# Performance work log

Measured on AMD Instinct MI355X. Metric: run time of the kernel, lower is better.

The kernel has to match this reference:

```python
import jax, jax.numpy as jnp
import numpy as np

N = 100000  # nodes
E = 1600000  # edges

def gcn_layer(x, W, b, src, tgt, ew):
    # support = x @ W + b ; messages gathered at src, weighted scatter-sum into tgt
    h = x @ W + b                      # [N, F_out]
    msg = h[src] * ew[:, None]         # [E, F_out]
    return jax.ops.segment_sum(msg, tgt, num_segments=N)  # [N, F_out]

def setup_inputs() -> dict:
    key = jax.random.key(0)
    ks = jax.random.split(key, 12)
    nfeat, nhid, nclass = 256, 128, 40
    x = jax.random.normal(ks[0], (N, nfeat), dtype=jnp.float32)
    src = jax.random.randint(ks[1], (E,), 0, N)
    tgt = jax.random.randint(ks[2], (E,), 0, N)
    edge_weight = jax.random.uniform(ks[3], (E,), dtype=jnp.float32)
    def w(k, fi, fo):
        return jax.random.normal(k, (fi, fo), dtype=jnp.float32) / np.sqrt(fi)
    return {
        "x": x, "src": src, "tgt": tgt, "edge_weight": edge_weight,
        "W0": w(ks[4], nfeat, nhid), "b0": jnp.zeros((nhid,), jnp.float32),
        "W1": w(ks[5], nhid, nhid),  "b1": jnp.zeros((nhid,), jnp.float32),
        "W2": w(ks[6], nhid, nhid),  "b2": jnp.zeros((nhid,), jnp.float32),
        "W3": w(ks[7], nhid, nclass),"b3": jnp.zeros((nclass,), jnp.float32),
    }

def reference(x, src, tgt, edge_weight, W0, b0, W1, b1, W2, b2, W3, b3):
    # RESK2 with nlayers=4, eval mode (dropout = identity).
    # x0 = relu(gc0); r = x0; x1 = relu(gc1); x2 = relu(gc2) + r; out = log_softmax(gc3)
    x0 = jax.nn.relu(gcn_layer(x, W0, b0, src, tgt, edge_weight))
    r = x0
    x1 = jax.nn.relu(gcn_layer(x0, W1, b1, src, tgt, edge_weight))
    x2 = jax.nn.relu(gcn_layer(x1, W2, b2, src, tgt, edge_weight)) + r
    logits = gcn_layer(x2, W3, b3, src, tgt, edge_weight)
    return jax.nn.log_softmax(logits, axis=1)
```

## Files before the change

kernel.cpp:

```cpp
#include <hip/hip_runtime.h>
#include <hip/hip_bf16.h>


typedef __attribute__((ext_vector_type(8))) short short8;
typedef __attribute__((ext_vector_type(4))) float float4v;

#define SC_SHIFT 8
#define SC_NODES 256
#define FILL_CAP 12288
#define SRC_MASK 0x1FFFF

static __device__ __forceinline__ float bf2f_lo(unsigned int v) {
    return __uint_as_float(v << 16);
}
static __device__ __forceinline__ float bf2f_hi(unsigned int v) {
    return __uint_as_float(v & 0xffff0000u);
}
static __device__ __forceinline__ unsigned short f2bf(float f) {
    unsigned int u = __float_as_uint(f);
    u = (u + 0x7fffu + ((u >> 16) & 1u)) >> 16;
    return (unsigned short)u;
}
static __device__ __forceinline__ unsigned int packbf(float a, float b) {
    return (unsigned int)f2bf(a) | ((unsigned int)f2bf(b) << 16);
}
static __device__ __forceinline__ float pw_w(unsigned int pe) {
    return __uint_as_float((pe >> 17) << 16);
}

static __device__ __forceinline__ void acc8(float* acc, uint4 v, float wt) {
    acc[0] = fmaf(bf2f_lo(v.x), wt, acc[0]);
    acc[1] = fmaf(bf2f_hi(v.x), wt, acc[1]);
    acc[2] = fmaf(bf2f_lo(v.y), wt, acc[2]);
    acc[3] = fmaf(bf2f_hi(v.y), wt, acc[3]);
    acc[4] = fmaf(bf2f_lo(v.z), wt, acc[4]);
    acc[5] = fmaf(bf2f_hi(v.z), wt, acc[5]);
    acc[6] = fmaf(bf2f_lo(v.w), wt, acc[6]);
    acc[7] = fmaf(bf2f_hi(v.w), wt, acc[7]);
}
static __device__ __forceinline__ void acc4(float* acc, uint2 v, float wt) {
    acc[0] = fmaf(bf2f_lo(v.x), wt, acc[0]);
    acc[1] = fmaf(bf2f_hi(v.x), wt, acc[1]);
    acc[2] = fmaf(bf2f_lo(v.y), wt, acc[2]);
    acc[3] = fmaf(bf2f_hi(v.y), wt, acc[3]);
}

__global__ __launch_bounds__(256) void k_count(const int* __restrict__ tgt,
                                               int* __restrict__ chunkTot,
                                               int E, int NSC) {
    __shared__ int hist[512];
    const int tid = threadIdx.x;
    hist[tid] = 0;
    hist[tid + 256] = 0;
    __syncthreads();
#pragma unroll
    for (int r = 0; r < 4; r++) {
        int e = blockIdx.x * 4096 + r * 1024 + tid * 4;
        if (e + 3 < E) {
            int4 tv = *(const int4*)&tgt[e];
            atomicAdd(&hist[tv.x >> SC_SHIFT], 1);
            atomicAdd(&hist[tv.y >> SC_SHIFT], 1);
            atomicAdd(&hist[tv.z >> SC_SHIFT], 1);
            atomicAdd(&hist[tv.w >> SC_SHIFT], 1);
        } else {
            for (int j = 0; j < 4; j++)
                if (e + j < E) atomicAdd(&hist[tgt[e + j] >> SC_SHIFT], 1);
        }
    }
    __syncthreads();
    for (int i = tid; i < NSC; i += 256) {
        int c = hist[i];
        if (c) atomicAdd(&chunkTot[i], c);
    }
}

__global__ __launch_bounds__(512) void k_scanB(const int* __restrict__ chunkTot,
                                               int* __restrict__ chunkStart,
                                               int* __restrict__ chunkCur,
                                               int E, int NSC) {
    __shared__ int sm[512];
    const int tid = threadIdx.x;
    int v = (tid < NSC) ? chunkTot[tid] : 0;
    sm[tid] = v;
    __syncthreads();
    for (int off = 1; off < 512; off <<= 1) {
        int t = (tid >= off) ? sm[tid - off] : 0;
        __syncthreads();
        sm[tid] += t;
        __syncthreads();
    }
    int excl = sm[tid] - v;
    if (tid < NSC) {
        chunkStart[tid] = excl;
        chunkCur[tid * 32] = excl;
    }
    if (tid == 0) chunkStart[NSC] = E;
}

__global__ __launch_bounds__(512) void k_bucket(const int* __restrict__ src,
                                                const int* __restrict__ tgt,
                                                const float* __restrict__ ew,
                                                int* __restrict__ chunkCur,
                                                unsigned int* __restrict__ st_pw,
                                                unsigned char* __restrict__ st_t8,
                                                int E) {
    __shared__ int cnt[512];
    __shared__ int rk[512];
    __shared__ int bbase[512];
    const int tid = threadIdx.x;
    cnt[tid] = 0;
    rk[tid] = 0;
    __syncthreads();

    int t16[16];
    unsigned int p16[16];
#pragma unroll
    for (int r = 0; r < 4; r++) {
        int e = blockIdx.x * 8192 + r * 2048 + tid * 4;
        if (e + 3 < E) {
            int4 tv = *(const int4*)&tgt[e];
            int4 sv = *(const int4*)&src[e];
            float4 wv = *(const float4*)&ew[e];
            t16[r * 4 + 0] = tv.x; t16[r * 4 + 1] = tv.y;
            t16[r * 4 + 2] = tv.z; t16[r * 4 + 3] = tv.w;
            p16[r * 4 + 0] = ((unsigned int)f2bf(wv.x) << 17) | (unsigned int)sv.x;
            p16[r * 4 + 1] = ((unsigned int)f2bf(wv.y) << 17) | (unsigned int)sv.y;
            p16[r * 4 + 2] = ((unsigned int)f2bf(wv.z) << 17) | (unsigned int)sv.z;
            p16[r * 4 + 3] = ((unsigned int)f2bf(wv.w) << 17) | (unsigned int)sv.w;
        } else {
            for (int j = 0; j < 4; j++) {
                int ee = e + j;
                t16[r * 4 + j] = (ee < E) ? tgt[ee] : -1;
                p16[r * 4 + j] = (ee < E)
                    ? (((unsigned int)f2bf(ew[ee]) << 17) | (unsigned int)src[ee])
                    : 0u;
            }
        }
    }
#pragma unroll
    for (int j = 0; j < 16; j++)
        if (t16[j] >= 0) atomicAdd(&cnt[t16[j] >> SC_SHIFT], 1);
    __syncthreads();
    {
        int c = cnt[tid];
        bbase[tid] = c ? atomicAdd(&chunkCur[tid * 32], c) : 0;
    }
    __syncthreads();
#pragma unroll
    for (int j = 0; j < 16; j++) {
        if (t16[j] >= 0) {
            int c = t16[j] >> SC_SHIFT;
            int pos = bbase[c] + atomicAdd(&rk[c], 1);
            st_pw[pos] = p16[j];
            st_t8[pos] = (unsigned char)(t16[j] & (SC_NODES - 1));
        }
    }
}

__global__ __launch_bounds__(256) void k_fill2(const unsigned int* __restrict__ st_pw,
                                               const unsigned char* __restrict__ st_t8,
                                               const int* __restrict__ chunkStart,
                                               int* __restrict__ rowptr,
                                               unsigned int* __restrict__ perm,
                                               int N, int E, int NSC) {
    __shared__ int lhist[SC_NODES];
    __shared__ int lcur[SC_NODES];
    __shared__ unsigned int ledge[FILL_CAP];
    const int tid = threadIdx.x;
    const int b = blockIdx.x;
    const int n0 = b << SC_SHIFT;
    const int nlocal = min(SC_NODES, N - n0);
    const int sstart = chunkStart[b];
    const int send = chunkStart[b + 1];
    const int cnt = send - sstart;

    lhist[tid] = 0;
    __syncthreads();
    for (int e = sstart + tid; e < send; e += 256)
        atomicAdd(&lhist[st_t8[e]], 1);
    __syncthreads();
    int v = lhist[tid];
    __syncthreads();
    lhist[tid] = v;
    __syncthreads();
    for (int off = 1; off < 256; off <<= 1) {
        int t = (tid >= off) ? lhist[tid - off] : 0;
        __syncthreads();
        lhist[tid] += t;
        __syncthreads();
    }
    int excl = lhist[tid] - v;
    if (tid < nlocal) rowptr[n0 + tid] = sstart + excl;
    if (b == NSC - 1 && tid == 0) rowptr[N] = E;
    lcur[tid] = excl;
    __syncthreads();

    if (cnt <= FILL_CAP) {
        for (int e = sstart + tid; e < send; e += 256) {
            int lt = st_t8[e];
            int pos = atomicAdd(&lcur[lt], 1);
            ledge[pos] = st_pw[e];
        }
        __syncthreads();
        for (int i = tid; i < cnt; i += 256) perm[sstart + i] = ledge[i];
    } else {
        for (int e = sstart + tid; e < send; e += 256) {
            int lt = st_t8[e];
            int pos = atomicAdd(&lcur[lt], 1);
            perm[sstart + pos] = st_pw[e];
        }
    }
}

__global__ __launch_bounds__(256) void k_wtrans_all(
    const float* __restrict__ W0, const float* __restrict__ W1,
    const float* __restrict__ W2, const float* __restrict__ W3,
    unsigned short* __restrict__ Wt0, unsigned short* __restrict__ Wt1,
    unsigned short* __restrict__ Wt2, unsigned short* __restrict__ Wt3,
    int* __restrict__ chunkTot) {
    int idx = blockIdx.x * 256 + threadIdx.x;
    if (idx < 512) chunkTot[idx] = 0;
    if (idx < 32768) {
        int c = idx >> 8, k = idx & 255;
        Wt0[idx] = f2bf(W0[k * 128 + c]);
    } else if (idx < 49152) {
        int i = idx - 32768;
        int c = i >> 7, k = i & 127;
        Wt1[i] = f2bf(W1[k * 128 + c]);
    } else if (idx < 65536) {
        int i = idx - 49152;
        int c = i >> 7, k = i & 127;
        Wt2[i] = f2bf(W2[k * 128 + c]);
    } else if (idx < 71680) {
        int i = idx - 65536;
        int c = i >> 7, k = i & 127;
        Wt3[i] = (c < 40) ? f2bf(W3[k * 40 + c]) : 0;
    }
}

template <int K, int AF32>
__global__ __launch_bounds__(256) void k_gemm_mfma(const void* __restrict__ Av,
                                                   const unsigned short* __restrict__ Wt,
                                                   const float* __restrict__ bias,
                                                   unsigned short* __restrict__ C, int N) {
    __shared__ union {
        struct {
            unsigned short As[64 * 40];
            unsigned short Bs[128 * 40];
        } s;
        unsigned short Cs[64 * 136];
    } u;
    __shared__ float bsh[128];
    const unsigned short* A16 = (const unsigned short*)Av;
    const float* A32 = (const float*)Av;
    const int tid = threadIdx.x;
    const int wave = tid >> 6, lane = tid & 63;
    const int quad = lane >> 4, l15 = lane & 15;
    const int rowBase = blockIdx.x * 64;

    if (tid < 128) bsh[tid] = bias[tid];

    const int r0 = tid >> 2, kc0 = tid & 3;
    const int rB1 = r0, rB2 = r0 + 64;
    int rg0 = rowBase + r0;
    rg0 = rg0 < N ? rg0 : N - 1;

    uint4 pa, pb0, pb1;
    auto load_step = [&](int k0) {
        if (AF32) {
            float4 f0 = *(const float4*)&A32[(size_t)rg0 * K + k0 + kc0 * 8];
            float4 f1 = *(const float4*)&A32[(size_t)rg0 * K + k0 + kc0 * 8 + 4];
            pa.x = packbf(f0.x, f0.y);
            pa.y = packbf(f0.z, f0.w);
            pa.z = packbf(f1.x, f1.y);
            pa.w = packbf(f1.z, f1.w);
        } else {
            pa = *(const uint4*)&A16[(size_t)rg0 * K + k0 + kc0 * 8];
        }
        pb0 = *(const uint4*)&Wt[(size_t)rB1 * K + k0 + kc0 * 8];
        pb1 = *(const uint4*)&Wt[(size_t)rB2 * K + k0 + kc0 * 8];
    };

    const float4v z = {0.f, 0.f, 0.f, 0.f};
    float4v acc[8];
#pragma unroll
    for (int j = 0; j < 8; j++) acc[j] = z;

    load_step(0);
    for (int k0 = 0; k0 < K; k0 += 32) {
        *(uint4*)&u.s.As[r0 * 40 + kc0 * 8] = pa;
        *(uint4*)&u.s.Bs[rB1 * 40 + kc0 * 8] = pb0;
        *(uint4*)&u.s.Bs[rB2 * 40 + kc0 * 8] = pb1;
        __syncthreads();
        if (k0 + 32 < K) load_step(k0 + 32);

        short8 a = *(const short8*)&u.s.As[(wave * 16 + l15) * 40 + quad * 8];
#pragma unroll
        for (int c = 0; c < 8; c++) {
            short8 b = *(const short8*)&u.s.Bs[(c * 16 + l15) * 40 + quad * 8];
            acc[c] = __builtin_amdgcn_mfma_f32_16x16x32_bf16(b, a, acc[c], 0, 0, 0);
        }
        __syncthreads();
    }

#pragma unroll
    for (int c = 0; c < 8; c++) {
        int colBase = c * 16 + quad * 4;
        float4 bv = *(const float4*)&bsh[colBase];
        uint2 o;
        o.x = packbf(acc[c][0] + bv.x, acc[c][1] + bv.y);
        o.y = packbf(acc[c][2] + bv.z, acc[c][3] + bv.w);
        *(uint2*)&u.Cs[(wave * 16 + l15) * 136 + colBase] = o;
    }
    __syncthreads();
#pragma unroll
    for (int i = 0; i < 4; i++) {
        int flat = i * 256 + tid;
        int row = flat >> 4, q = flat & 15;
        int grow = rowBase + row;
        if (grow < N) {
            uint4 v = *(const uint4*)&u.Cs[row * 136 + q * 8];
            *(uint4*)&C[(size_t)grow * 128 + q * 8] = v;
        }
    }
}

__global__ __launch_bounds__(256) void k_gemm40_mfma(const unsigned short* __restrict__ A,
                                                     const unsigned short* __restrict__ Wt3,
                                                     const float* __restrict__ bias,
                                                     unsigned short* __restrict__ C, int N) {
    __shared__ union {
        struct {
            unsigned short As[64 * 40];
            unsigned short Bs[48 * 136];
        } s;
        unsigned short Cs[64 * 72];
    } u;
    __shared__ float bsh[64];
    const int tid = threadIdx.x;
    const int wave = tid >> 6, lane = tid & 63;
    const int quad = lane >> 4, l15 = lane & 15;
    const int rowBase = blockIdx.x * 64;

    if (tid < 64) bsh[tid] = (tid < 40) ? bias[tid] : 0.f;

    const int r0 = tid >> 2, kc0 = tid & 3;
    int rg0 = rowBase + r0;
    rg0 = rg0 < N ? rg0 : N - 1;

    for (int t = tid; t < 48 * 16; t += 256) {
        int r = t >> 4, kc = t & 15;
        uint4 v = *(const uint4*)&Wt3[r * 128 + kc * 8];
        *(uint4*)&u.s.Bs[r * 136 + kc * 8] = v;
    }

    uint4 pa;
    auto load_step = [&](int k0) {
        pa = *(const uint4*)&A[(size_t)rg0 * 128 + k0 + kc0 * 8];
    };

    const float4v z = {0.f, 0.f, 0.f, 0.f};
    float4v acc[3];
#pragma unroll
    for (int j = 0; j < 3; j++) acc[j] = z;

    load_step(0);
    for (int k0 = 0; k0 < 128; k0 += 32) {
        *(uint4*)&u.s.As[r0 * 40 + kc0 * 8] = pa;
        __syncthreads();
        if (k0 + 32 < 128) load_step(k0 + 32);

        short8 a = *(const short8*)&u.s.As[(wave * 16 + l15) * 40 + quad * 8];
#pragma unroll
        for (int c = 0; c < 3; c++) {
            short8 b = *(const short8*)&u.s.Bs[(c * 16 + l15) * 136 + k0 + quad * 8];
            acc[c] = __builtin_amdgcn_mfma_f32_16x16x32_bf16(b, a, acc[c], 0, 0, 0);
        }
        __syncthreads();
    }

#pragma unroll
    for (int c = 0; c < 4; c++) {
        int colBase = c * 16 + quad * 4;
        uint2 o;
        if (c < 3) {
            float4 bv = *(const float4*)&bsh[colBase];
            o.x = packbf(acc[c][0] + bv.x, acc[c][1] + bv.y);
            o.y = packbf(acc[c][2] + bv.z, acc[c][3] + bv.w);
        } else {
            o.x = 0u;
            o.y = 0u;
        }
        *(uint2*)&u.Cs[(wave * 16 + l15) * 72 + colBase] = o;
    }
    __syncthreads();
#pragma unroll
    for (int i = 0; i < 2; i++) {
        int flat = i * 256 + tid;
        int row = flat >> 3, q = flat & 7;
        int grow = rowBase + row;
        if (grow < N) {
            uint4 v = *(const uint4*)&u.Cs[row * 72 + q * 8];
            *(uint4*)&C[(size_t)grow * 64 + q * 8] = v;
        }
    }
}

__global__ __launch_bounds__(256) void k_agg128(const unsigned short* __restrict__ h,
                                                const int* __restrict__ rowptr,
                                                const unsigned int* __restrict__ perm,
                                                const unsigned short* __restrict__ resid,
                                                unsigned short* __restrict__ out, int N) {
    int node = (blockIdx.x * 256 + threadIdx.x) >> 6;
    if (node >= N) return;
    const int lane = threadIdx.x & 63;
    const int g = lane >> 4, l = lane & 15;
    const int beg = rowptr[node], end = rowptr[node + 1];
    const int last = end - 1;

    float acc[8] = {};
    for (int base = beg; base < end; base += 16) {
        int e0 = base + g, e1 = base + 4 + g, e2 = base + 8 + g, e3 = base + 12 + g;
        unsigned int p0 = perm[e0 <= last ? e0 : last];
        unsigned int p1 = perm[e1 <= last ? e1 : last];
        unsigned int p2 = perm[e2 <= last ? e2 : last];
        unsigned int p3 = perm[e3 <= last ? e3 : last];
        uint4 a0 = *(const uint4*)&h[(size_t)(p0 & SRC_MASK) * 128 + l * 8];
        uint4 a1 = *(const uint4*)&h[(size_t)(p1 & SRC_MASK) * 128 + l * 8];
        uint4 a2 = *(const uint4*)&h[(size_t)(p2 & SRC_MASK) * 128 + l * 8];
        uint4 a3 = *(const uint4*)&h[(size_t)(p3 & SRC_MASK) * 128 + l * 8];
        float w0 = e0 <= last ? pw_w(p0) : 0.f;
        float w1 = e1 <= last ? pw_w(p1) : 0.f;
        float w2 = e2 <= last ? pw_w(p2) : 0.f;
        float w3 = e3 <= last ? pw_w(p3) : 0.f;
        acc8(acc, a0, w0);
        acc8(acc, a1, w1);
        acc8(acc, a2, w2);
        acc8(acc, a3, w3);
    }

#pragma unroll
    for (int i = 0; i < 8; i++) {
        acc[i] += __shfl_xor(acc[i], 16);
        acc[i] += __shfl_xor(acc[i], 32);
    }

    if (g == 0) {
#pragma unroll
        for (int i = 0; i < 8; i++) acc[i] = fmaxf(acc[i], 0.f);
        if (resid) {
            uint4 rv = *(const uint4*)&resid[(size_t)node * 128 + l * 8];
            acc[0] += bf2f_lo(rv.x); acc[1] += bf2f_hi(rv.x);
            acc[2] += bf2f_lo(rv.y); acc[3] += bf2f_hi(rv.y);
            acc[4] += bf2f_lo(rv.z); acc[5] += bf2f_hi(rv.z);
            acc[6] += bf2f_lo(rv.w); acc[7] += bf2f_hi(rv.w);
        }
        uint4 o;
        o.x = packbf(acc[0], acc[1]);
        o.y = packbf(acc[2], acc[3]);
        o.z = packbf(acc[4], acc[5]);
        o.w = packbf(acc[6], acc[7]);
        *(uint4*)&out[(size_t)node * 128 + l * 8] = o;
    }
}

__global__ __launch_bounds__(256) void k_agg40_lsm(const unsigned short* __restrict__ h,
                                                   const int* __restrict__ rowptr,
                                                   const unsigned int* __restrict__ perm,
                                                   float* __restrict__ out, int N) {
    int node = (blockIdx.x * 256 + threadIdx.x) >> 6;
    if (node >= N) return;
    const int lane = threadIdx.x & 63;
    const int g = lane >> 4, l = lane & 15;
    const int beg = rowptr[node], end = rowptr[node + 1];
    const int last = end - 1;
    const int lc = l < 10 ? l : 0;

    float acc[4] = {};
    for (int base = beg; base < end; base += 16) {
        int e0 = base + g, e1 = base + 4 + g, e2 = base + 8 + g, e3 = base + 12 + g;
        unsigned int p0 = perm[e0 <= last ? e0 : last];
        unsigned int p1 = perm[e1 <= last ? e1 : last];
        unsigned int p2 = perm[e2 <= last ? e2 : last];
        unsigned int p3 = perm[e3 <= last ? e3 : last];
        uint2 a0 = *(const uint2*)&h[(size_t)(p0 & SRC_MASK) * 64 + lc * 4];
        uint2 a1 = *(const uint2*)&h[(size_t)(p1 & SRC_MASK) * 64 + lc * 4];
        uint2 a2 = *(const uint2*)&h[(size_t)(p2 & SRC_MASK) * 64 + lc * 4];
        uint2 a3 = *(const uint2*)&h[(size_t)(p3 & SRC_MASK) * 64 + lc * 4];
        float w0 = e0 <= last ? pw_w(p0) : 0.f;
        float w1 = e1 <= last ? pw_w(p1) : 0.f;
        float w2 = e2 <= last ? pw_w(p2) : 0.f;
        float w3 = e3 <= last ? pw_w(p3) : 0.f;
        acc4(acc, a0, w0);
        acc4(acc, a1, w1);
        acc4(acc, a2, w2);
        acc4(acc, a3, w3);
    }
#pragma unroll
    for (int i = 0; i < 4; i++) {
        acc[i] += __shfl_xor(acc[i], 16);
        acc[i] += __shfl_xor(acc[i], 32);
    }

    bool vf = l < 10;
    float m = vf ? fmaxf(fmaxf(acc[0], acc[1]), fmaxf(acc[2], acc[3]))
                 : -__builtin_inff();
#pragma unroll
    for (int off = 1; off < 16; off <<= 1) m = fmaxf(m, __shfl_xor(m, off));
    float s = vf ? (expf(acc[0] - m) + expf(acc[1] - m) +
                    expf(acc[2] - m) + expf(acc[3] - m))
                 : 0.f;
#pragma unroll
    for (int off = 1; off < 16; off <<= 1) s += __shfl_xor(s, off);
    float ls = m + logf(s);
    if (g == 0 && vf) {
        float4 o = make_float4(acc[0] - ls, acc[1] - ls, acc[2] - ls, acc[3] - ls);
        *(float4*)&out[(size_t)node * 40 + l * 4] = o;
    }
}

extern "C" void kernel_launch(void* const* d_in, const int* in_sizes, int n_in,
                              void* d_out, int out_size, void* d_ws, size_t ws_size,
                              hipStream_t stream) {
    const float* x  = (const float*)d_in[0];
    const int*   src = (const int*)d_in[1];
    const int*   tgt = (const int*)d_in[2];
    const float* ew  = (const float*)d_in[3];
    const float* W0 = (const float*)d_in[4];
    const float* b0 = (const float*)d_in[5];
    const float* W1 = (const float*)d_in[6];
    const float* b1 = (const float*)d_in[7];
    const float* W2 = (const float*)d_in[8];
    const float* b2 = (const float*)d_in[9];
    const float* W3 = (const float*)d_in[10];
    const float* b3 = (const float*)d_in[11];

    const int N = in_sizes[0] / 256;
    const int E = in_sizes[1];
    const int NSC = (N + SC_NODES - 1) >> SC_SHIFT;

    char* ws = (char*)d_ws;
    size_t off = 0;
    auto alloc = [&](size_t bytes) -> void* {
        void* p = ws + off;
        off = (off + bytes + 255) & ~(size_t)255;
        return p;
    };
    unsigned short* XCb = (unsigned short*)alloc((size_t)N * 128 * 2);
    size_t hbytes = (size_t)N * 128 * 2;
    size_t sbytes = (size_t)E * 5 + 256;
    char* hbuf = (char*)alloc(hbytes > sbytes ? hbytes : sbytes);
    unsigned short* Hb = (unsigned short*)hbuf;
    unsigned int* st_pw = (unsigned int*)hbuf;
    unsigned char* st_t8 = (unsigned char*)(hbuf + (size_t)E * 4);
    char* buf1 = (char*)alloc((size_t)N * 128 * 2);
    unsigned short* XAb  = (unsigned short*)buf1;
    unsigned short* H40b = (unsigned short*)buf1;
    unsigned short* XBb  = (unsigned short*)alloc((size_t)N * 128 * 2);
    int*   rowptr    = (int*)alloc((size_t)(N + 1) * 4);
    int*   chunkTot  = (int*)alloc(512 * 4);
    int*   chunkStart= (int*)alloc(520 * 4);
    int*   chunkCur  = (int*)alloc(512 * 32 * 4);
    unsigned int* perm = (unsigned int*)alloc((size_t)E * 4);
    unsigned short* Wt0 = (unsigned short*)alloc(256 * 128 * 2);
    unsigned short* Wt1 = (unsigned short*)alloc(128 * 128 * 2);
    unsigned short* Wt2 = (unsigned short*)alloc(128 * 128 * 2);
    unsigned short* Wt3 = (unsigned short*)alloc(48 * 128 * 2);
    (void)ws_size;

    float* logits = (float*)d_out;

    k_wtrans_all<<<(71680 + 255) / 256, 256, 0, stream>>>(W0, W1, W2, W3,
                                                          Wt0, Wt1, Wt2, Wt3,
                                                          chunkTot);
    k_count<<<(E + 4095) / 4096, 256, 0, stream>>>(tgt, chunkTot, E, NSC);
    k_scanB<<<1, 512, 0, stream>>>(chunkTot, chunkStart, chunkCur, E, NSC);
    k_bucket<<<(E + 8191) / 8192, 512, 0, stream>>>(src, tgt, ew, chunkCur,
                                                    st_pw, st_t8, E);
    k_fill2<<<NSC, 256, 0, stream>>>(st_pw, st_t8, chunkStart, rowptr, perm,
                                     N, E, NSC);

    const int gGemm = (N + 63) / 64;
    const int gWave = (N + 3) / 4;

    k_gemm_mfma<256, 1><<<gGemm, 256, 0, stream>>>(x, Wt0, b0, Hb, N);
    k_agg128<<<gWave, 256, 0, stream>>>(Hb, rowptr, perm, nullptr, XAb, N);
    k_gemm_mfma<128, 0><<<gGemm, 256, 0, stream>>>(XAb, Wt1, b1, Hb, N);
    k_agg128<<<gWave, 256, 0, stream>>>(Hb, rowptr, perm, nullptr, XBb, N);
    k_gemm_mfma<128, 0><<<gGemm, 256, 0, stream>>>(XBb, Wt2, b2, Hb, N);
    k_agg128<<<gWave, 256, 0, stream>>>(Hb, rowptr, perm, XAb, XCb, N);
    k_gemm40_mfma<<<gGemm, 256, 0, stream>>>(XCb, Wt3, b3, H40b, N);
    k_agg40_lsm<<<gWave, 256, 0, stream>>>(H40b, rowptr, perm, logits, N);
}
```

Baseline: 490.6 us.

## Pad CSR rows to multiples of 16 and use bf16 dot2 accumulation

Each node's edge list in the CSR is now padded to a multiple of 16 with zero entries, which encode weight 0 and source 0. Begin and end pointers are stored separately so the aggregation kernels can load four edge entries with one 128-bit load and drop the per-edge bounds clamping and selects. The per-element multiply is also replaced by the bf16 dot2 builtin, which pairs each feature with its weight in a single instruction. In exchange, perm becomes larger, padded entries gather row 0 and waste bandwidth, and k_fill2 gains a zero-fill pass. The weight is kept in bf16 as before.

Result: no change. 490.7 us (+0.0%).

```diff
diff --git a/kernel.cpp b/kernel.cpp
--- a/kernel.cpp
+++ b/kernel.cpp
@@ -4,10 +4,18 @@
 
 typedef __attribute__((ext_vector_type(8))) short short8;
 typedef __attribute__((ext_vector_type(4))) float float4v;
+
+#if defined(__has_builtin)
+#if __has_builtin(__builtin_amdgcn_fdot2_f32_bf16)
+#define HAVE_DOT2 1
+typedef __attribute__((ext_vector_type(2))) __bf16 bf16x2;
+#endif
+#endif
 
 #define SC_SHIFT 8
 #define SC_NODES 256
 #define FILL_CAP 12288
+#define PAD_HEADROOM 4096
 #define SRC_MASK 0x1FFFF
 
 static __device__ __forceinline__ float bf2f_lo(unsigned int v) {
@@ -24,25 +32,35 @@
 static __device__ __forceinline__ unsigned int packbf(float a, float b) {
     return (unsigned int)f2bf(a) | ((unsigned int)f2bf(b) << 16);
 }
-static __device__ __forceinline__ float pw_w(unsigned int pe) {
-    return __uint_as_float((pe >> 17) << 16);
-}
-
-static __device__ __forceinline__ void acc8(float* acc, uint4 v, float wt) {
-    acc[0] = fmaf(bf2f_lo(v.x), wt, acc[0]);
-    acc[1] = fmaf(bf2f_hi(v.x), wt, acc[1]);
-    acc[2] = fmaf(bf2f_lo(v.y), wt, acc[2]);
-    acc[3] = fmaf(bf2f_hi(v.y), wt, acc[3]);
-    acc[4] = fmaf(bf2f_lo(v.z), wt, acc[4]);
-    acc[5] = fmaf(bf2f_hi(v.z), wt, acc[5]);
-    acc[6] = fmaf(bf2f_lo(v.w), wt, acc[6]);
-    acc[7] = fmaf(bf2f_hi(v.w), wt, acc[7]);
-}
-static __device__ __forceinline__ void acc4(float* acc, uint2 v, float wt) {
-    acc[0] = fmaf(bf2f_lo(v.x), wt, acc[0]);
-    acc[1] = fmaf(bf2f_hi(v.x), wt, acc[1]);
-    acc[2] = fmaf(bf2f_lo(v.y), wt, acc[2]);
-    acc[3] = fmaf(bf2f_hi(v.y), wt, acc[3]);
+
+static __device__ __forceinline__ float dotp(unsigned int h2, unsigned int w2,
+                                             float acc) {
+#ifdef HAVE_DOT2
+    return __builtin_amdgcn_fdot2_f32_bf16(__builtin_bit_cast(bf16x2, h2),
+                                           __builtin_bit_cast(bf16x2, w2), acc,
+                                           false);
+#else
+    return fmaf(bf2f_lo(h2), bf2f_lo(w2), fmaf(bf2f_hi(h2), bf2f_hi(w2), acc));
+#endif
+}
+
+static __device__ __forceinline__ void acc8p(float* acc, uint4 v,
+                                             unsigned int wlo, unsigned int whi) {
+    acc[0] = dotp(v.x, wlo, acc[0]);
+    acc[1] = dotp(v.x, whi, acc[1]);
+    acc[2] = dotp(v.y, wlo, acc[2]);
+    acc[3] = dotp(v.y, whi, acc[3]);
+    acc[4] = dotp(v.z, wlo, acc[4]);
+    acc[5] = dotp(v.z, whi, acc[5]);
+    acc[6] = dotp(v.w, wlo, acc[6]);
+    acc[7] = dotp(v.w, whi, acc[7]);
+}
+static __device__ __forceinline__ void acc4p(float* acc, uint2 v,
+                                             unsigned int wlo, unsigned int whi) {
+    acc[0] = dotp(v.x, wlo, acc[0]);
+    acc[1] = dotp(v.x, whi, acc[1]);
+    acc[2] = dotp(v.y, wlo, acc[2]);
+    acc[3] = dotp(v.y, whi, acc[3]);
 }
 
 __global__ __launch_bounds__(256) void k_count(const int* __restrict__ tgt,
@@ -160,10 +178,11 @@
 __global__ __launch_bounds__(256) void k_fill2(const unsigned int* __restrict__ st_pw,
                                                const unsigned char* __restrict__ st_t8,
                                                const int* __restrict__ chunkStart,
-                                               int* __restrict__ rowptr,
+                                               int* __restrict__ rowBeg,
+                                               int* __restrict__ rowEnd,
                                                unsigned int* __restrict__ perm,
-                                               int N, int E, int NSC) {
-    __shared__ int lhist[SC_NODES];
+                                               int N, int NSC) {
+    __shared__ int lsc[SC_NODES];
     __shared__ int lcur[SC_NODES];
     __shared__ unsigned int ledge[FILL_CAP];
     const int tid = threadIdx.x;
@@ -172,42 +191,50 @@
     const int nlocal = min(SC_NODES, N - n0);
     const int sstart = chunkStart[b];
     const int send = chunkStart[b + 1];
-    const int cnt = send - sstart;
-
-    lhist[tid] = 0;
+    const int pstart = (sstart + b * PAD_HEADROOM + 15) & ~15;
+
+    lsc[tid] = 0;
     __syncthreads();
     for (int e = sstart + tid; e < send; e += 256)
-        atomicAdd(&lhist[st_t8[e]], 1);
-    __syncthreads();
-    int v = lhist[tid];
-    __syncthreads();
-    lhist[tid] = v;
+        atomicAdd(&lsc[st_t8[e]], 1);
+    __syncthreads();
+    int deg = lsc[tid];
+    int pdeg = (deg + 15) & ~15;
+    __syncthreads();
+    lsc[tid] = pdeg;
     __syncthreads();
     for (int off = 1; off < 256; off <<= 1) {
-        int t = (tid >= off) ? lhist[tid - off] : 0;
-        __syncthreads();
-        lhist[tid] += t;
-        __syncthreads();
-    }
-    int excl = lhist[tid] - v;
-    if (tid < nlocal) rowptr[n0 + tid] = sstart + excl;
-    if (b == NSC - 1 && tid == 0) rowptr[N] = E;
-    lcur[tid] = excl;
-    __syncthreads();
-
-    if (cnt <= FILL_CAP) {
+        int t = (tid >= off) ? lsc[tid - off] : 0;
+        __syncthreads();
+        lsc[tid] += t;
+        __syncthreads();
+    }
+    const int ptotal = lsc[SC_NODES - 1];
+    int pexcl = lsc[tid] - pdeg;
+    if (tid < nlocal) {
+        rowBeg[n0 + tid] = pstart + pexcl;
+        rowEnd[n0 + tid] = pstart + pexcl + pdeg;
+    }
+    lcur[tid] = pexcl;
+    __syncthreads();
+
+    if (ptotal <= FILL_CAP) {
+        for (int i = tid; i < ptotal; i += 256) ledge[i] = 0u;
+        __syncthreads();
         for (int e = sstart + tid; e < send; e += 256) {
             int lt = st_t8[e];
             int pos = atomicAdd(&lcur[lt], 1);
             ledge[pos] = st_pw[e];
         }
         __syncthreads();
-        for (int i = tid; i < cnt; i += 256) perm[sstart + i] = ledge[i];
+        for (int i = tid; i < ptotal; i += 256) perm[pstart + i] = ledge[i];
     } else {
+        for (int i = tid; i < ptotal; i += 256) perm[pstart + i] = 0u;
+        __syncthreads();
         for (int e = sstart + tid; e < send; e += 256) {
             int lt = st_t8[e];
             int pos = atomicAdd(&lcur[lt], 1);
-            perm[sstart + pos] = st_pw[e];
+            perm[pstart + pos] = st_pw[e];
         }
     }
 }
@@ -407,7 +434,8 @@
 }
 
 __global__ __launch_bounds__(256) void k_agg128(const unsigned short* __restrict__ h,
-                                                const int* __restrict__ rowptr,
+                                                const int* __restrict__ rowBeg,
+                                                const int* __restrict__ rowEnd,
                                                 const unsigned int* __restrict__ perm,
                                                 const unsigned short* __restrict__ resid,
                                                 unsigned short* __restrict__ out, int N) {
@@ -415,28 +443,23 @@
     if (node >= N) return;
     const int lane = threadIdx.x & 63;
     const int g = lane >> 4, l = lane & 15;
-    const int beg = rowptr[node], end = rowptr[node + 1];
-    const int last = end - 1;
+    const int beg = rowBeg[node], end = rowEnd[node];
 
     float acc[8] = {};
     for (int base = beg; base < end; base += 16) {
-        int e0 = base + g, e1 = base + 4 + g, e2 = base + 8 + g, e3 = base + 12 + g;
-        unsigned int p0 = perm[e0 <= last ? e0 : last];
-        unsigned int p1 = perm[e1 <= last ? e1 : last];
-        unsigned int p2 = perm[e2 <= last ? e2 : last];
-        unsigned int p3 = perm[e3 <= last ? e3 : last];
-        uint4 a0 = *(const uint4*)&h[(size_t)(p0 & SRC_MASK) * 128 + l * 8];
-        uint4 a1 = *(const uint4*)&h[(size_t)(p1 & SRC_MASK) * 128 + l * 8];
-        uint4 a2 = *(const uint4*)&h[(size_t)(p2 & SRC_MASK) * 128 + l * 8];
-        uint4 a3 = *(const uint4*)&h[(size_t)(p3 & SRC_MASK) * 128 + l * 8];
-        float w0 = e0 <= last ? pw_w(p0) : 0.f;
-        float w1 = e1 <= last ? pw_w(p1) : 0.f;
-        float w2 = e2 <= last ? pw_w(p2) : 0.f;
-        float w3 = e3 <= last ? pw_w(p3) : 0.f;
-        acc8(acc, a0, w0);
-        acc8(acc, a1, w1);
-        acc8(acc, a2, w2);
-        acc8(acc, a3, w3);
+        uint4 pv = *(const uint4*)&perm[base + g * 4];
+        unsigned int wl0 = pv.x >> 17, wh0 = wl0 << 16;
+        unsigned int wl1 = pv.y >> 17, wh1 = wl1 << 16;
+        unsigned int wl2 = pv.z >> 17, wh2 = wl2 << 16;
+        unsigned int wl3 = pv.w >> 17, wh3 = wl3 << 16;
+        uint4 a0 = *(const uint4*)&h[(size_t)(pv.x & SRC_MASK) * 128 + l * 8];
+        uint4 a1 = *(const uint4*)&h[(size_t)(pv.y & SRC_MASK) * 128 + l * 8];
+        uint4 a2 = *(const uint4*)&h[(size_t)(pv.z & SRC_MASK) * 128 + l * 8];
+        uint4 a3 = *(const uint4*)&h[(size_t)(pv.w & SRC_MASK) * 128 + l * 8];
+        acc8p(acc, a0, wl0, wh0);
+        acc8p(acc, a1, wl1, wh1);
+        acc8p(acc, a2, wl2, wh2);
+        acc8p(acc, a3, wl3, wh3);
     }
 
 #pragma unroll
@@ -465,36 +488,32 @@
 }
 
 __global__ __launch_bounds__(256) void k_agg40_lsm(const unsigned short* __restrict__ h,
-                                                   const int* __restrict__ rowptr,
+                                                   const int* __restrict__ rowBeg,
+                                                   const int* __restrict__ rowEnd,
                                                    const unsigned int* __restrict__ perm,
                                                    float* __restrict__ out, int N) {
     int node = (blockIdx.x * 256 + threadIdx.x) >> 6;
     if (node >= N) return;
     const int lane = threadIdx.x & 63;
     const int g = lane >> 4, l = lane & 15;
-    const int beg = rowptr[node], end = rowptr[node + 1];
-    const int last = end - 1;
+    const int beg = rowBeg[node], end = rowEnd[node];
     const int lc = l < 10 ? l : 0;
 
     float acc[4] = {};
     for (int base = beg; base < end; base += 16) {
-        int e0 = base + g, e1 = base + 4 + g, e2 = base + 8 + g, e3 = base + 12 + g;
-        unsigned int p0 = perm[e0 <= last ? e0 : last];
-        unsigned int p1 = perm[e1 <= last ? e1 : last];
-        unsigned int p2 = perm[e2 <= last ? e2 : last];
-        unsigned int p3 = perm[e3 <= last ? e3 : last];
-        uint2 a0 = *(const uint2*)&h[(size_t)(p0 & SRC_MASK) * 64 + lc * 4];
-        uint2 a1 = *(const uint2*)&h[(size_t)(p1 & SRC_MASK) * 64 + lc * 4];
-        uint2 a2 = *(const uint2*)&h[(size_t)(p2 & SRC_MASK) * 64 + lc * 4];
-        uint2 a3 = *(const uint2*)&h[(size_t)(p3 & SRC_MASK) * 64 + lc * 4];
-        float w0 = e0 <= last ? pw_w(p0) : 0.f;
-        float w1 = e1 <= last ? pw_w(p1) : 0.f;
-        float w2 = e2 <= last ? pw_w(p2) : 0.f;
-        float w3 = e3 <= last ? pw_w(p3) : 0.f;
-        acc4(acc, a0, w0);
-        acc4(acc, a1, w1);
-        acc4(acc, a2, w2);
-        acc4(acc, a3, w3);
+        uint4 pv = *(const uint4*)&perm[base + g * 4];
+        unsigned int wl0 = pv.x >> 17, wh0 = wl0 << 16;
+        unsigned int wl1 = pv.y >> 17, wh1 = wl1 << 16;
+        unsigned int wl2 = pv.z >> 17, wh2 = wl2 << 16;
+        unsigned int wl3 = pv.w >> 17, wh3 = wl3 << 16;
+        uint2 a0 = *(const uint2*)&h[(size_t)(pv.x & SRC_MASK) * 64 + lc * 4];
+        uint2 a1 = *(const uint2*)&h[(size_t)(pv.y & SRC_MASK) * 64 + lc * 4];
+        uint2 a2 = *(const uint2*)&h[(size_t)(pv.z & SRC_MASK) * 64 + lc * 4];
+        uint2 a3 = *(const uint2*)&h[(size_t)(pv.w & SRC_MASK) * 64 + lc * 4];
+        acc4p(acc, a0, wl0, wh0);
+        acc4p(acc, a1, wl1, wh1);
+        acc4p(acc, a2, wl2, wh2);
+        acc4p(acc, a3, wl3, wh3);
     }
 #pragma unroll
     for (int i = 0; i < 4; i++) {
@@ -557,11 +576,12 @@
     unsigned short* XAb  = (unsigned short*)buf1;
     unsigned short* H40b = (unsigned short*)buf1;
     unsigned short* XBb  = (unsigned short*)alloc((size_t)N * 128 * 2);
-    int*   rowptr    = (int*)alloc((size_t)(N + 1) * 4);
+    int*   rowBeg    = (int*)alloc((size_t)(N + 1) * 4);
+    int*   rowEnd    = (int*)alloc((size_t)(N + 1) * 4);
     int*   chunkTot  = (int*)alloc(512 * 4);
     int*   chunkStart= (int*)alloc(520 * 4);
     int*   chunkCur  = (int*)alloc(512 * 32 * 4);
-    unsigned int* perm = (unsigned int*)alloc((size_t)E * 4);
+    unsigned int* perm = (unsigned int*)alloc(((size_t)E + (size_t)(NSC + 1) * PAD_HEADROOM) * 4);
     unsigned short* Wt0 = (unsigned short*)alloc(256 * 128 * 2);
     unsigned short* Wt1 = (unsigned short*)alloc(128 * 128 * 2);
     unsigned short* Wt2 = (unsigned short*)alloc(128 * 128 * 2);
@@ -577,18 +597,18 @@
     k_scanB<<<1, 512, 0, stream>>>(chunkTot, chunkStart, chunkCur, E, NSC);
     k_bucket<<<(E + 8191) / 8192, 512, 0, stream>>>(src, tgt, ew, chunkCur,
                                                     st_pw, st_t8, E);
-    k_fill2<<<NSC, 256, 0, stream>>>(st_pw, st_t8, chunkStart, rowptr, perm,
-                                     N, E, NSC);
+    k_fill2<<<NSC, 256, 0, stream>>>(st_pw, st_t8, chunkStart, rowBeg, rowEnd,
+                                     perm, N, NSC);
 
     const int gGemm = (N + 63) / 64;
     const int gWave = (N + 3) / 4;
 
     k_gemm_mfma<256, 1><<<gGemm, 256, 0, stream>>>(x, Wt0, b0, Hb, N);
-    k_agg128<<<gWave, 256, 0, stream>>>(Hb, rowptr, perm, nullptr, XAb, N);
+    k_agg128<<<gWave, 256, 0, stream>>>(Hb, rowBeg, rowEnd, perm, nullptr, XAb, N);
     k_gemm_mfma<128, 0><<<gGemm, 256, 0, stream>>>(XAb, Wt1, b1, Hb, N);
-    k_agg128<<<gWave, 256, 0, stream>>>(Hb, rowptr, perm, nullptr, XBb, N);
+    k_agg128<<<gWave, 256, 0, stream>>>(Hb, rowBeg, rowEnd, perm, nullptr, XBb, N);
     k_gemm_mfma<128, 0><<<gGemm, 256, 0, stream>>>(XBb, Wt2, b2, Hb, N);
-    k_agg128<<<gWave, 256, 0, stream>>>(Hb, rowptr, perm, XAb, XCb, N);
+    k_agg128<<<gWave, 256, 0, stream>>>(Hb, rowBeg, rowEnd, perm, XAb, XCb, N);
     k_gemm40_mfma<<<gGemm, 256, 0, stream>>>(XCb, Wt3, b3, H40b, N);
-    k_agg40_lsm<<<gWave, 256, 0, stream>>>(H40b, rowptr, perm, logits, N);
-}
+    k_agg40_lsm<<<gWave, 256, 0, stream>>>(H40b, rowBeg, rowEnd, perm, logits, N);
+}
```
